# Performance work log

Hardware: AMD Instinct MI355X
Metric: run time of the kernel (lower is better)

The kernel has to match this reference:

```python
import jax, jax.numpy as jnp
import numpy as np

B, SQ, SK, H, NH = 2, 2048, 2048, 1024, 16
HD = H // NH  # 64


def setup_inputs() -> dict:
    key = jax.random.key(0)
    ks = jax.random.split(key, 12)
    s = 1.0 / np.sqrt(H)
    inp = {
        "query": jax.random.normal(ks[0], (B, SQ, H), jnp.float32),
        "key": jax.random.normal(ks[1], (B, SK, H), jnp.float32),
        "value": jax.random.normal(ks[2], (B, SK, H), jnp.float32),
        # lower-triangular causal mask [B, SQ, SK]; nonzero = attend
        "causal_mask": jnp.broadcast_to(
            jnp.tril(jnp.ones((SQ, SK), jnp.int32)), (B, SQ, SK)
        ),
        "Wq": jax.random.uniform(ks[3], (H, H), jnp.float32, -s, s),
        "bq": jnp.zeros((H,), jnp.float32),
        "Wk": jax.random.uniform(ks[4], (H, H), jnp.float32, -s, s),
        "bk": jnp.zeros((H,), jnp.float32),
        "Wv": jax.random.uniform(ks[5], (H, H), jnp.float32, -s, s),
        "bv": jnp.zeros((H,), jnp.float32),
        "Wo": jax.random.uniform(ks[6], (H, H), jnp.float32, -s, s),
        "bo": jnp.zeros((H,), jnp.float32),
        "ln_g": jnp.ones((H,), jnp.float32),
        "ln_b": jnp.zeros((H,), jnp.float32),
    }
    return inp


def _layer_norm(x, g, b, eps=1e-5):
    mu = jnp.mean(x, axis=-1, keepdims=True)
    var = jnp.var(x, axis=-1, keepdims=True)
    return (x - mu) * jax.lax.rsqrt(var + eps) * g + b


def reference(query, key, value, causal_mask, Wq, bq, Wk, bk, Wv, bv, Wo, bo, ln_g, ln_b):
    # projections (torch Linear: x @ W.T + b)
    q = (query @ Wq.T + bq).reshape(B, SQ, NH, HD)
    k = (key @ Wk.T + bk).reshape(B, SK, NH, HD)
    v = (value @ Wv.T + bv).reshape(B, SK, NH, HD)
    # scores [B, NH, SQ, SK]
    scores = jnp.einsum("bqhd,bkhd->bhqk", q, k) / np.sqrt(HD).astype(np.float32)
    scores = jnp.where(causal_mask[:, None, :, :] == 0, -jnp.inf, scores)
    attn = jax.nn.softmax(scores, axis=-1)
    # dropout is identity in eval mode
    out = jnp.einsum("bhqk,bkhd->bqhd", attn, v).reshape(B, SQ, H)
    out = out @ Wo.T + bo
    return _layer_norm(query + out, ln_g, ln_b)
```

## Files before the change

### kernel.cpp

```cpp
#include <hip/hip_runtime.h>
#include <hip/hip_bf16.h>

#define SQL 2048
#define SKL 2048
#define HH  1024
#define NHH 16
#define HDD 64
#define BB  2
#define MM  (BB*SQL)

typedef __attribute__((ext_vector_type(8))) short short8;
typedef __attribute__((ext_vector_type(4))) float f32x4;
typedef unsigned short u16;

__device__ inline u16 f2bf(float f) {
    unsigned int u = __float_as_uint(f);
    u += 0x7fffu + ((u >> 16) & 1u);
    return (u16)(u >> 16);
}

__device__ inline unsigned int cvt_pk_bf16(float lo, float hi) {
    unsigned int r;
    asm("v_cvt_pk_bf16_f32 %0, %1, %2" : "=v"(r) : "v"(lo), "v"(hi));
    return r;
}

__device__ inline void gl_lds16(const void* g, void* l) {
    __builtin_amdgcn_global_load_lds(
        (const __attribute__((address_space(1))) unsigned int*)g,
        (__attribute__((address_space(3))) unsigned int*)l, 16, 0, 0);
}

__global__ __launch_bounds__(256) void cvt_all_kernel(
    const float* __restrict__ q, const float* __restrict__ k, const float* __restrict__ v,
    const float* __restrict__ wq, const float* __restrict__ wk,
    const float* __restrict__ wv, const float* __restrict__ wo,
    u16* __restrict__ xq, u16* __restrict__ xk, u16* __restrict__ xv,
    u16* __restrict__ wqb, u16* __restrict__ wkb, u16* __restrict__ wvb, u16* __restrict__ wob)
{
    int b = blockIdx.x;
    const float* src; u16* dst;
    if      (b < 4096)  { src = q;  dst = xq; }
    else if (b < 8192)  { src = k;  dst = xk;  b -= 4096; }
    else if (b < 12288) { src = v;  dst = xv;  b -= 8192; }
    else if (b < 13312) { src = wq; dst = wqb; b -= 12288; }
    else if (b < 14336) { src = wk; dst = wkb; b -= 13312; }
    else if (b < 15360) { src = wv; dst = wvb; b -= 14336; }
    else                { src = wo; dst = wob; b -= 15360; }
    int i = (b * 256 + threadIdx.x) * 4;
    float4 vv = *(const float4*)(src + i);
    unsigned int d0 = cvt_pk_bf16(vv.x, vv.y);
    unsigned int d1 = cvt_pk_bf16(vv.z, vv.w);
    *(uint2*)(dst + i) = make_uint2(d0, d1);
}

__global__ __launch_bounds__(256) void proj_kernel(
    const u16* __restrict__ xq, const u16* __restrict__ xk, const u16* __restrict__ xv,
    const u16* __restrict__ wqb, const u16* __restrict__ wkb, const u16* __restrict__ wvb,
    const float* __restrict__ bq, const float* __restrict__ bk, const float* __restrict__ bv,
    u16* __restrict__ oq, u16* __restrict__ ok, u16* __restrict__ ov)
{
    const int z = blockIdx.z;
    const u16* A      = (z == 0) ? xq  : (z == 1) ? xk  : xv;
    const u16* W      = (z == 0) ? wqb : (z == 1) ? wkb : wvb;
    const float* bias = (z == 0) ? bq  : (z == 1) ? bk  : bv;
    u16* outb         = (z == 0) ? oq  : (z == 1) ? ok  : ov;
    const float scale = (z == 0) ? 0.125f * 1.4426950408889634f : 1.0f;

    __shared__ u16 lds_a[128 * 32];
    __shared__ u16 lds_b[128 * 32];

    const int t = threadIdx.x;
    const int lane = t & 63;
    const int quad = lane >> 4;
    const int lo = lane & 15;
    const int wv = t >> 6;
    const int wm = (wv >> 1) * 64, wn = (wv & 1) * 64;
    const int m0 = blockIdx.x * 128;
    const int n0 = blockIdx.y * 128;

    f32x4 acc[4][4];
#pragma unroll
    for (int i = 0; i < 4; i++)
#pragma unroll
        for (int j = 0; j < 4; j++) acc[i][j] = (f32x4){0.f, 0.f, 0.f, 0.f};

    const int sl0 = t, sl1 = 256 + t;
    const int r0 = sl0 >> 2, c0 = ((sl0 & 3) ^ ((r0 >> 1) & 3)) * 8;
    const int r1 = sl1 >> 2, c1 = ((sl1 & 3) ^ ((r1 >> 1) & 3)) * 8;

    for (int k0 = 0; k0 < HH; k0 += 32) {
        gl_lds16(A + (size_t)(m0 + r0) * HH + k0 + c0, &lds_a[sl0 * 8]);
        gl_lds16(A + (size_t)(m0 + r1) * HH + k0 + c1, &lds_a[sl1 * 8]);
        gl_lds16(W + (size_t)(n0 + r0) * HH + k0 + c0, &lds_b[sl0 * 8]);
        gl_lds16(W + (size_t)(n0 + r1) * HH + k0 + c1, &lds_b[sl1 * 8]);
        __syncthreads();
        short8 af[4], bf[4];
#pragma unroll
        for (int i = 0; i < 4; i++) {
            const int ra = wm + i * 16 + lo;
            const int rb = wn + i * 16 + lo;
            af[i] = *(const short8*)&lds_a[ra * 32 + ((quad ^ ((ra >> 1) & 3)) * 8)];
            bf[i] = *(const short8*)&lds_b[rb * 32 + ((quad ^ ((rb >> 1) & 3)) * 8)];
        }
        if (z == 2) {
#pragma unroll
            for (int i = 0; i < 4; i++)
#pragma unroll
                for (int j = 0; j < 4; j++)
                    acc[i][j] = __builtin_amdgcn_mfma_f32_16x16x32_bf16(bf[j], af[i], acc[i][j], 0, 0, 0);
        } else {
#pragma unroll
            for (int i = 0; i < 4; i++)
#pragma unroll
                for (int j = 0; j < 4; j++)
                    acc[i][j] = __builtin_amdgcn_mfma_f32_16x16x32_bf16(af[i], bf[j], acc[i][j], 0, 0, 0);
        }
        __syncthreads();
    }

#pragma unroll
    for (int i = 0; i < 4; i++) {
#pragma unroll
        for (int j = 0; j < 4; j++) {
#pragma unroll
            for (int r = 0; r < 4; r++) {
                if (z == 2) {
                    int dg  = n0 + wn + j * 16 + quad * 4 + r;
                    int tok = m0 + wm + i * 16 + lo;
                    float val = acc[i][j][r] + bias[dg];
                    int head = dg >> 6, d = dg & 63;
                    int bi = tok >> 11, s = tok & 2047;
                    outb[(((size_t)bi * NHH + head) * HDD + d) * SKL + s] = f2bf(val);
                } else {
                    int row = m0 + wm + i * 16 + quad * 4 + r;
                    int col = n0 + wn + j * 16 + lo;
                    float val = (acc[i][j][r] + bias[col]) * scale;
                    int bi = row >> 11, s = row & 2047;
                    int head = col >> 6, d = col & 63;
                    outb[(((size_t)bi * NHH + head) * SQL + s) * HDD + d] = f2bf(val);
                }
            }
        }
    }
}

__global__ __launch_bounds__(256) void outproj_kernel(
    const u16* __restrict__ A, const u16* __restrict__ W,
    const float* __restrict__ bias, const float* __restrict__ resid,
    float* __restrict__ outf)
{
    __shared__ u16 lds_a[128 * 32];
    __shared__ u16 lds_b[128 * 32];

    const int t = threadIdx.x;
    const int lane = t & 63;
    const int quad = lane >> 4;
    const int lo = lane & 15;
    const int wv = t >> 6;
    const int wm = (wv >> 1) * 64, wn = (wv & 1) * 64;
    const int m0 = blockIdx.x * 128;
    const int n0 = blockIdx.y * 128;

    f32x4 acc[4][4];
#pragma unroll
    for (int i = 0; i < 4; i++)
#pragma unroll
        for (int j = 0; j < 4; j++) acc[i][j] = (f32x4){0.f, 0.f, 0.f, 0.f};

    const int sl0 = t, sl1 = 256 + t;
    const int r0 = sl0 >> 2, c0 = ((sl0 & 3) ^ ((r0 >> 1) & 3)) * 8;
    const int r1 = sl1 >> 2, c1 = ((sl1 & 3) ^ ((r1 >> 1) & 3)) * 8;

    for (int k0 = 0; k0 < HH; k0 += 32) {
        gl_lds16(A + (size_t)(m0 + r0) * HH + k0 + c0, &lds_a[sl0 * 8]);
        gl_lds16(A + (size_t)(m0 + r1) * HH + k0 + c1, &lds_a[sl1 * 8]);
        gl_lds16(W + (size_t)(n0 + r0) * HH + k0 + c0, &lds_b[sl0 * 8]);
        gl_lds16(W + (size_t)(n0 + r1) * HH + k0 + c1, &lds_b[sl1 * 8]);
        __syncthreads();
        short8 af[4], bf[4];
#pragma unroll
        for (int i = 0; i < 4; i++) {
            const int ra = wm + i * 16 + lo;
            const int rb = wn + i * 16 + lo;
            af[i] = *(const short8*)&lds_a[ra * 32 + ((quad ^ ((ra >> 1) & 3)) * 8)];
            bf[i] = *(const short8*)&lds_b[rb * 32 + ((quad ^ ((rb >> 1) & 3)) * 8)];
        }
#pragma unroll
        for (int i = 0; i < 4; i++)
#pragma unroll
            for (int j = 0; j < 4; j++)
                acc[i][j] = __builtin_amdgcn_mfma_f32_16x16x32_bf16(af[i], bf[j], acc[i][j], 0, 0, 0);
        __syncthreads();
    }

#pragma unroll
    for (int i = 0; i < 4; i++)
#pragma unroll
        for (int j = 0; j < 4; j++)
#pragma unroll
            for (int r = 0; r < 4; r++) {
                int row = m0 + wm + i * 16 + quad * 4 + r;
                int col = n0 + wn + j * 16 + lo;
                float val = acc[i][j][r] + bias[col] + resid[(size_t)row * HH + col];
                outf[(size_t)row * HH + col] = val;
            }
}

#define PSTR 72

__global__ __launch_bounds__(256) void attn_kernel(
    const u16* __restrict__ qb, const u16* __restrict__ kb, const u16* __restrict__ vtb,
    u16* __restrict__ attn_out)
{
    __shared__ u16 k_lds[64 * 64];
    __shared__ u16 vt_lds[64 * 64];
    __shared__ u16 p_lds[4 * 16 * PSTR];

    const int t = threadIdx.x;
    const int lane = t & 63;
    const int quad = lane >> 4;
    const int lo = lane & 15;
    const int w = t >> 6;
    const int qt = (SQL / 64 - 1) - (blockIdx.x >> 5);
    const int bh = blockIdx.x & 31;
    const int q0 = qt * 64;

    const u16* qbase = qb + ((size_t)bh * SQL + q0 + w * 16 + lo) * HDD + quad * 8;
    short8 qf0 = *(const short8*)qbase;
    short8 qf1 = *(const short8*)(qbase + 32);

    float m_s = -__builtin_inff(), l_s = 0.f;
    f32x4 o[4];
#pragma unroll
    for (int j = 0; j < 4; j++) o[j] = (f32x4){0.f, 0.f, 0.f, 0.f};

    const int sl0 = t, sl1 = 256 + t;
    const int r0 = sl0 >> 3, c0 = ((sl0 & 7) ^ (r0 & 7)) * 8;
    const int r1 = sl1 >> 3, c1 = ((sl1 & 7) ^ (r1 & 7)) * 8;
    const u16* kbh = kb + (size_t)bh * SKL * HDD;
    const u16* vbh = vtb + (size_t)bh * HDD * SKL;
    u16* ppriv = &p_lds[w * 16 * PSTR];

    for (int kt = 0; kt <= qt; kt++) {
        const int k0 = kt * 64;
        gl_lds16(kbh + (size_t)(k0 + r0) * HDD + c0, &k_lds[sl0 * 8]);
        gl_lds16(kbh + (size_t)(k0 + r1) * HDD + c1, &k_lds[sl1 * 8]);
        gl_lds16(vbh + (size_t)r0 * SKL + k0 + c0, &vt_lds[sl0 * 8]);
        gl_lds16(vbh + (size_t)r1 * SKL + k0 + c1, &vt_lds[sl1 * 8]);
        __syncthreads();

        f32x4 s[4];
        __builtin_amdgcn_s_setprio(1);
#pragma unroll
        for (int nt = 0; nt < 4; nt++) {
            const int row = nt * 16 + lo;
            short8 kf0 = *(const short8*)&k_lds[row * 64 + ((quad ^ (row & 7)) * 8)];
            short8 kf1 = *(const short8*)&k_lds[row * 64 + (((4 + quad) ^ (row & 7)) * 8)];
            s[nt] = (f32x4){0.f, 0.f, 0.f, 0.f};
            s[nt] = __builtin_amdgcn_mfma_f32_16x16x32_bf16(kf0, qf0, s[nt], 0, 0, 0);
            s[nt] = __builtin_amdgcn_mfma_f32_16x16x32_bf16(kf1, qf1, s[nt], 0, 0, 0);
        }
        __builtin_amdgcn_s_setprio(0);
        if (kt == qt) {
            const int ql = w * 16 + lo;
#pragma unroll
            for (int nt = 0; nt < 4; nt++)
#pragma unroll
                for (int r = 0; r < 4; r++)
                    if (nt * 16 + quad * 4 + r > ql) s[nt][r] = -__builtin_inff();
        }

        float mx = s[0][0];
#pragma unroll
        for (int nt = 0; nt < 4; nt++)
#pragma unroll
            for (int r = 0; r < 4; r++) mx = fmaxf(mx, s[nt][r]);
        mx = fmaxf(mx, __shfl_xor(mx, 16));
        mx = fmaxf(mx, __shfl_xor(mx, 32));

        if (!__all(mx - m_s <= 8.0f)) {
            float mnew = fmaxf(m_s, mx);
            float al = __builtin_amdgcn_exp2f(m_s - mnew);
            m_s = mnew;
            l_s *= al;
            float alr[4];
#pragma unroll
            for (int r = 0; r < 4; r++) alr[r] = __shfl(al, quad * 4 + r, 16);
#pragma unroll
            for (int nt = 0; nt < 4; nt++)
#pragma unroll
                for (int r = 0; r < 4; r++) o[nt][r] *= alr[r];
        }

        float rs = 0.f;
#pragma unroll
        for (int nt = 0; nt < 4; nt++)
#pragma unroll
            for (int r = 0; r < 4; r++) {
                s[nt][r] = __builtin_amdgcn_exp2f(s[nt][r] - m_s);
                rs += s[nt][r];
            }
        rs += __shfl_xor(rs, 16);
        rs += __shfl_xor(rs, 32);
        l_s += rs;

#pragma unroll
        for (int nt = 0; nt < 4; nt++) {
            unsigned int d0 = cvt_pk_bf16(s[nt][0], s[nt][1]);
            unsigned int d1 = cvt_pk_bf16(s[nt][2], s[nt][3]);
            *(uint2*)&ppriv[lo * PSTR + nt * 16 + quad * 4] = make_uint2(d0, d1);
        }
        short8 pf0 = *(const short8*)&ppriv[lo * PSTR + quad * 8];
        short8 pf1 = *(const short8*)&ppriv[lo * PSTR + 32 + quad * 8];

        __builtin_amdgcn_s_setprio(1);
#pragma unroll
        for (int nt = 0; nt < 4; nt++) {
            const int row = nt * 16 + lo;
            short8 vf0 = *(const short8*)&vt_lds[row * 64 + ((quad ^ (row & 7)) * 8)];
            short8 vf1 = *(const short8*)&vt_lds[row * 64 + (((4 + quad) ^ (row & 7)) * 8)];
            o[nt] = __builtin_amdgcn_mfma_f32_16x16x32_bf16(pf0, vf0, o[nt], 0, 0, 0);
            o[nt] = __builtin_amdgcn_mfma_f32_16x16x32_bf16(pf1, vf1, o[nt], 0, 0, 0);
        }
        __builtin_amdgcn_s_setprio(0);
        __syncthreads();
    }

    const int b = bh >> 4, h = bh & 15;
    float inv[4];
#pragma unroll
    for (int r = 0; r < 4; r++) inv[r] = 1.0f / __shfl(l_s, quad * 4 + r, 16);
#pragma unroll
    for (int nt = 0; nt < 4; nt++)
#pragma unroll
        for (int r = 0; r < 4; r++) {
            int srow = q0 + w * 16 + quad * 4 + r;
            attn_out[((size_t)b * SQL + srow) * HH + h * HDD + nt * 16 + lo] =
                f2bf(o[nt][r] * inv[r]);
        }
}

__global__ __launch_bounds__(256) void ln_kernel(const float* __restrict__ x,
                                                 const float* __restrict__ g,
                                                 const float* __restrict__ bb,
                                                 float* __restrict__ out)
{
    const int row = blockIdx.x;
    const int t = threadIdx.x;
    const float* xr = x + (size_t)row * HH;
    float4 v = *(const float4*)(xr + t * 4);
    float s1 = v.x + v.y + v.z + v.w;
    float s2 = v.x * v.x + v.y * v.y + v.z * v.z + v.w * v.w;
#pragma unroll
    for (int off = 32; off; off >>= 1) { s1 += __shfl_xor(s1, off); s2 += __shfl_xor(s2, off); }
    __shared__ float red[8];
    if ((t & 63) == 0) { red[(t >> 6) * 2] = s1; red[(t >> 6) * 2 + 1] = s2; }
    __syncthreads();
    s1 = red[0] + red[2] + red[4] + red[6];
    s2 = red[1] + red[3] + red[5] + red[7];
    float mu = s1 * (1.0f / HH);
    float var = s2 * (1.0f / HH) - mu * mu;
    float rstd = rsqrtf(var + 1e-5f);
    float4 gg = *(const float4*)(g + t * 4);
    float4 b4 = *(const float4*)(bb + t * 4);
    float4 o;
    o.x = (v.x - mu) * rstd * gg.x + b4.x;
    o.y = (v.y - mu) * rstd * gg.y + b4.y;
    o.z = (v.z - mu) * rstd * gg.z + b4.z;
    o.w = (v.w - mu) * rstd * gg.w + b4.w;
    *(float4*)(out + (size_t)row * HH + t * 4) = o;
}

extern "C" void kernel_launch(void* const* d_in, const int* in_sizes, int n_in,
                              void* d_out, int out_size, void* d_ws, size_t ws_size,
                              hipStream_t stream)
{
    const float* query = (const float*)d_in[0];
    const float* key   = (const float*)d_in[1];
    const float* value = (const float*)d_in[2];
    const float* Wq = (const float*)d_in[4];
    const float* bq = (const float*)d_in[5];
    const float* Wk = (const float*)d_in[6];
    const float* bk = (const float*)d_in[7];
    const float* Wv = (const float*)d_in[8];
    const float* bv = (const float*)d_in[9];
    const float* Wo = (const float*)d_in[10];
    const float* bo = (const float*)d_in[11];
    const float* ln_g = (const float*)d_in[12];
    const float* ln_b = (const float*)d_in[13];
    float* out = (float*)d_out;

    char* wp = (char*)d_ws;
    auto alloc = [&](size_t bytes) { void* p = (void*)wp; wp += (bytes + 255) & ~(size_t)255; return p; };
    const int nW = HH * HH;
    const int nX = MM * HH;
    u16* wqb = (u16*)alloc((size_t)nW * 2);
    u16* wkb = (u16*)alloc((size_t)nW * 2);
    u16* wvb = (u16*)alloc((size_t)nW * 2);
    u16* wob = (u16*)alloc((size_t)nW * 2);
    u16* xq  = (u16*)alloc((size_t)nX * 2);
    u16* xk  = (u16*)alloc((size_t)nX * 2);
    u16* xv  = (u16*)alloc((size_t)nX * 2);
    u16* qbuf = (u16*)alloc((size_t)nX * 2);
    u16* kbuf = (u16*)alloc((size_t)nX * 2);
    u16* vbuf = (u16*)alloc((size_t)nX * 2);
    u16* attnb = (u16*)alloc((size_t)nX * 2);
    float* projf = (float*)alloc((size_t)nX * 4);

    cvt_all_kernel<<<16384, 256, 0, stream>>>(query, key, value, Wq, Wk, Wv, Wo,
                                              xq, xk, xv, wqb, wkb, wvb, wob);

    proj_kernel<<<dim3(32, 8, 3), 256, 0, stream>>>(
        xq, xk, xv, wqb, wkb, wvb, bq, bk, bv, qbuf, kbuf, vbuf);

    attn_kernel<<<1024, 256, 0, stream>>>(qbuf, kbuf, vbuf, attnb);

    outproj_kernel<<<dim3(32, 8), 256, 0, stream>>>(attnb, wob, bo, query, projf);

    ln_kernel<<<MM, 256, 0, stream>>>(projf, ln_g, ln_b, out);
}
```

Before: 280.6 us.

## Double-buffer LDS in projection GEMMs and use software bf16 rounding

The input and output projection GEMMs now use two LDS buffers per operand. The next K-tile's global-to-LDS load is issued before the MFMAs on the current tile, which should hide load latency and drop one barrier per iteration. Separately, the v_cvt_pk_bf16_f32 inline asm is replaced by a software round-to-nearest-even bf16 conversion, both in the convert kernel and in the attention P packing. That adds ALU instructions in the attention inner loop and doubles LDS use in the GEMMs, which may lower occupancy. Because the prefetch is asynchronous and is only fenced by the barrier at the end of the iteration, correctness depends on the vmcnt wait that barrier places.

```diff
diff --git a/kernel.cpp b/kernel.cpp
--- a/kernel.cpp
+++ b/kernel.cpp
@@ -10,6 +10,7 @@
 #define MM  (BB*SQL)
 
 typedef __attribute__((ext_vector_type(8))) short short8;
+typedef __attribute__((ext_vector_type(4))) short short4v;
 typedef __attribute__((ext_vector_type(4))) float f32x4;
 typedef unsigned short u16;
 
@@ -17,12 +18,6 @@
     unsigned int u = __float_as_uint(f);
     u += 0x7fffu + ((u >> 16) & 1u);
     return (u16)(u >> 16);
-}
-
-__device__ inline unsigned int cvt_pk_bf16(float lo, float hi) {
-    unsigned int r;
-    asm("v_cvt_pk_bf16_f32 %0, %1, %2" : "=v"(r) : "v"(lo), "v"(hi));
-    return r;
 }
 
 __device__ inline void gl_lds16(const void* g, void* l) {
@@ -49,9 +44,9 @@
     else                { src = wo; dst = wob; b -= 15360; }
     int i = (b * 256 + threadIdx.x) * 4;
     float4 vv = *(const float4*)(src + i);
-    unsigned int d0 = cvt_pk_bf16(vv.x, vv.y);
-    unsigned int d1 = cvt_pk_bf16(vv.z, vv.w);
-    *(uint2*)(dst + i) = make_uint2(d0, d1);
+    ushort4 oo;
+    oo.x = f2bf(vv.x); oo.y = f2bf(vv.y); oo.z = f2bf(vv.z); oo.w = f2bf(vv.w);
+    *(ushort4*)(dst + i) = oo;
 }
 
 __global__ __launch_bounds__(256) void proj_kernel(
@@ -67,8 +62,8 @@
     u16* outb         = (z == 0) ? oq  : (z == 1) ? ok  : ov;
     const float scale = (z == 0) ? 0.125f * 1.4426950408889634f : 1.0f;
 
-    __shared__ u16 lds_a[128 * 32];
-    __shared__ u16 lds_b[128 * 32];
+    __shared__ u16 lds_a[2][128 * 32];
+    __shared__ u16 lds_b[2][128 * 32];
 
     const int t = threadIdx.x;
     const int lane = t & 63;
@@ -89,19 +84,28 @@
     const int r0 = sl0 >> 2, c0 = ((sl0 & 3) ^ ((r0 >> 1) & 3)) * 8;
     const int r1 = sl1 >> 2, c1 = ((sl1 & 3) ^ ((r1 >> 1) & 3)) * 8;
 
+    gl_lds16(A + (size_t)(m0 + r0) * HH + c0, &lds_a[0][sl0 * 8]);
+    gl_lds16(A + (size_t)(m0 + r1) * HH + c1, &lds_a[0][sl1 * 8]);
+    gl_lds16(W + (size_t)(n0 + r0) * HH + c0, &lds_b[0][sl0 * 8]);
+    gl_lds16(W + (size_t)(n0 + r1) * HH + c1, &lds_b[0][sl1 * 8]);
+    __syncthreads();
+
+    int cur = 0;
     for (int k0 = 0; k0 < HH; k0 += 32) {
-        gl_lds16(A + (size_t)(m0 + r0) * HH + k0 + c0, &lds_a[sl0 * 8]);
-        gl_lds16(A + (size_t)(m0 + r1) * HH + k0 + c1, &lds_a[sl1 * 8]);
-        gl_lds16(W + (size_t)(n0 + r0) * HH + k0 + c0, &lds_b[sl0 * 8]);
-        gl_lds16(W + (size_t)(n0 + r1) * HH + k0 + c1, &lds_b[sl1 * 8]);
-        __syncthreads();
+        if (k0 + 32 < HH) {
+            const int kn = k0 + 32;
+            gl_lds16(A + (size_t)(m0 + r0) * HH + kn + c0, &lds_a[cur ^ 1][sl0 * 8]);
+            gl_lds16(A + (size_t)(m0 + r1) * HH + kn + c1, &lds_a[cur ^ 1][sl1 * 8]);
+            gl_lds16(W + (size_t)(n0 + r0) * HH + kn + c0, &lds_b[cur ^ 1][sl0 * 8]);
+            gl_lds16(W + (size_t)(n0 + r1) * HH + kn + c1, &lds_b[cur ^ 1][sl1 * 8]);
+        }
         short8 af[4], bf[4];
 #pragma unroll
         for (int i = 0; i < 4; i++) {
             const int ra = wm + i * 16 + lo;
             const int rb = wn + i * 16 + lo;
-            af[i] = *(const short8*)&lds_a[ra * 32 + ((quad ^ ((ra >> 1) & 3)) * 8)];
-            bf[i] = *(const short8*)&lds_b[rb * 32 + ((quad ^ ((rb >> 1) & 3)) * 8)];
+            af[i] = *(const short8*)&lds_a[cur][ra * 32 + ((quad ^ ((ra >> 1) & 3)) * 8)];
+            bf[i] = *(const short8*)&lds_b[cur][rb * 32 + ((quad ^ ((rb >> 1) & 3)) * 8)];
         }
         if (z == 2) {
 #pragma unroll
@@ -117,6 +121,7 @@
                     acc[i][j] = __builtin_amdgcn_mfma_f32_16x16x32_bf16(af[i], bf[j], acc[i][j], 0, 0, 0);
         }
         __syncthreads();
+        cur ^= 1;
     }
 
 #pragma unroll
@@ -150,8 +155,8 @@
     const float* __restrict__ bias, const float* __restrict__ resid,
     float* __restrict__ outf)
 {
-    __shared__ u16 lds_a[128 * 32];
-    __shared__ u16 lds_b[128 * 32];
+    __shared__ u16 lds_a[2][128 * 32];
+    __shared__ u16 lds_b[2][128 * 32];
 
     const int t = threadIdx.x;
     const int lane = t & 63;
@@ -172,19 +177,28 @@
     const int r0 = sl0 >> 2, c0 = ((sl0 & 3) ^ ((r0 >> 1) & 3)) * 8;
     const int r1 = sl1 >> 2, c1 = ((sl1 & 3) ^ ((r1 >> 1) & 3)) * 8;
 
+    gl_lds16(A + (size_t)(m0 + r0) * HH + c0, &lds_a[0][sl0 * 8]);
+    gl_lds16(A + (size_t)(m0 + r1) * HH + c1, &lds_a[0][sl1 * 8]);
+    gl_lds16(W + (size_t)(n0 + r0) * HH + c0, &lds_b[0][sl0 * 8]);
+    gl_lds16(W + (size_t)(n0 + r1) * HH + c1, &lds_b[0][sl1 * 8]);
+    __syncthreads();
+
+    int cur = 0;
     for (int k0 = 0; k0 < HH; k0 += 32) {
-        gl_lds16(A + (size_t)(m0 + r0) * HH + k0 + c0, &lds_a[sl0 * 8]);
-        gl_lds16(A + (size_t)(m0 + r1) * HH + k0 + c1, &lds_a[sl1 * 8]);
-        gl_lds16(W + (size_t)(n0 + r0) * HH + k0 + c0, &lds_b[sl0 * 8]);
-        gl_lds16(W + (size_t)(n0 + r1) * HH + k0 + c1, &lds_b[sl1 * 8]);
-        __syncthreads();
+        if (k0 + 32 < HH) {
+            const int kn = k0 + 32;
+            gl_lds16(A + (size_t)(m0 + r0) * HH + kn + c0, &lds_a[cur ^ 1][sl0 * 8]);
+            gl_lds16(A + (size_t)(m0 + r1) * HH + kn + c1, &lds_a[cur ^ 1][sl1 * 8]);
+            gl_lds16(W + (size_t)(n0 + r0) * HH + kn + c0, &lds_b[cur ^ 1][sl0 * 8]);
+            gl_lds16(W + (size_t)(n0 + r1) * HH + kn + c1, &lds_b[cur ^ 1][sl1 * 8]);
+        }
         short8 af[4], bf[4];
 #pragma unroll
         for (int i = 0; i < 4; i++) {
             const int ra = wm + i * 16 + lo;
             const int rb = wn + i * 16 + lo;
-            af[i] = *(const short8*)&lds_a[ra * 32 + ((quad ^ ((ra >> 1) & 3)) * 8)];
-            bf[i] = *(const short8*)&lds_b[rb * 32 + ((quad ^ ((rb >> 1) & 3)) * 8)];
+            af[i] = *(const short8*)&lds_a[cur][ra * 32 + ((quad ^ ((ra >> 1) & 3)) * 8)];
+            bf[i] = *(const short8*)&lds_b[cur][rb * 32 + ((quad ^ ((rb >> 1) & 3)) * 8)];
         }
 #pragma unroll
         for (int i = 0; i < 4; i++)
@@ -192,6 +206,7 @@
             for (int j = 0; j < 4; j++)
                 acc[i][j] = __builtin_amdgcn_mfma_f32_16x16x32_bf16(af[i], bf[j], acc[i][j], 0, 0, 0);
         __syncthreads();
+        cur ^= 1;
     }
 
 #pragma unroll
@@ -307,9 +322,10 @@
 
 #pragma unroll
         for (int nt = 0; nt < 4; nt++) {
-            unsigned int d0 = cvt_pk_bf16(s[nt][0], s[nt][1]);
-            unsigned int d1 = cvt_pk_bf16(s[nt][2], s[nt][3]);
-            *(uint2*)&ppriv[lo * PSTR + nt * 16 + quad * 4] = make_uint2(d0, d1);
+            short4v pk;
+#pragma unroll
+            for (int r = 0; r < 4; r++) pk[r] = (short)f2bf(s[nt][r]);
+            *(short4v*)&ppriv[lo * PSTR + nt * 16 + quad * 4] = pk;
         }
         short8 pf0 = *(const short8*)&ppriv[lo * PSTR + quad * 8];
         short8 pf1 = *(const short8*)&ppriv[lo * PSTR + 32 + quad * 8];
```

After: 294.0 us. 1.05x slower.
